# Optimization experiments

Measured on AMD Instinct MI355X. Metric: run time of the kernel, lower is better.

The kernel has to match this reference:

```python
import jax, jax.numpy as jnp
import numpy as np

N_NODES = 100000
N_EDGES = 1600000
IN_CH = 128
OUT_CH = 128


def setup_inputs() -> dict:
    key = jax.random.key(0)
    k1, k2, k3 = jax.random.split(key, 3)
    x = jax.random.normal(k1, (N_NODES, IN_CH), dtype=jnp.float32)
    edge_index = jax.random.randint(k2, (2, N_EDGES), 0, N_NODES, dtype=jnp.int64)
    # glorot-like init for the linear weight, stored as [in, out]
    W = jax.random.normal(k3, (IN_CH, OUT_CH), dtype=jnp.float32) * (2.0 / (IN_CH + OUT_CH)) ** 0.5
    bias = jnp.zeros((OUT_CH,), dtype=jnp.float32)
    return {"x": x, "edge_index": edge_index, "W": W, "bias": bias}


def reference(x, edge_index, W, bias):
    N = x.shape[0]
    # linear transform (bias-free, matches Linear(in, out, bias=False))
    h = x @ W  # [N, out]

    # add self loops (improved=False -> fill_value = 1.0)
    loop = jnp.arange(N, dtype=edge_index.dtype)
    src = jnp.concatenate([edge_index[0], loop])
    dst = jnp.concatenate([edge_index[1], loop])
    ew = jnp.ones(src.shape[0], dtype=h.dtype)  # edge_weight None -> ones

    # symmetric GCN normalization: deg from dst, norm = d^-1/2[src] * w * d^-1/2[dst]
    deg = jax.ops.segment_sum(ew, dst, num_segments=N)
    deg_inv_sqrt = jnp.where(deg > 0, jax.lax.rsqrt(deg), 0.0)
    w = deg_inv_sqrt[src] * ew * deg_inv_sqrt[dst]

    # spmm aggregation: out[dst] += w * h[src]
    out = jax.ops.segment_sum(h[src] * w[:, None], dst, num_segments=N)
    return out + bias
```

## Files before the change

kernel.cpp:

```cpp
#include <hip/hip_runtime.h>
#include <hip/hip_bf16.h>

constexpr int kNodes = 100000;
constexpr int kEdges = 1600000;
constexpr int kCh    = 128;
constexpr int kCap   = 32;
constexpr int kOvfCap = 8192;
constexpr int kPartSize = kNodes / 8;
constexpr int kFillBlocks = 512;
constexpr int kGemmBlocks = (kNodes + 127) / 128;

typedef __attribute__((ext_vector_type(8))) short short8;
typedef __attribute__((ext_vector_type(4))) float floatx4;
typedef __attribute__((ext_vector_type(4))) int   intx4;
typedef __attribute__((ext_vector_type(2))) float floatx2;


__global__ __launch_bounds__(512) void k_fused(const float* __restrict__ x,
                                               const float* __restrict__ W,
                                               const int* __restrict__ srcArr,
                                               const int* __restrict__ dstArr,
                                               int* __restrict__ cnt,
                                               int* __restrict__ bucket,
                                               int* __restrict__ ovfCnt,
                                               int* __restrict__ ovfD,
                                               int* __restrict__ ovfS,
                                               __hip_bfloat16* __restrict__ hs) {
  if (blockIdx.x < kFillBlocks) {
    int part = blockIdx.x & 7;
    int bip  = blockIdx.x >> 3;
    int lo = part * kPartSize;
    const intx4* d4 = (const intx4*)dstArr;
    const intx4* s4 = (const intx4*)srcArr;
    for (int i = bip * 512 + (int)threadIdx.x; i < kEdges / 4; i += (kFillBlocks >> 3) * 512) {
      intx4 dv = __builtin_nontemporal_load(d4 + i);
      intx4 sv = __builtin_nontemporal_load(s4 + i);
      #pragma unroll
      for (int k = 0; k < 4; k++) {
        int d = dv[k];
        if ((unsigned)(d - lo) < (unsigned)kPartSize) {
          int pos = atomicAdd(&cnt[d], 1);
          if (pos < kCap) {
            bucket[(long)d * kCap + pos] = sv[k];
          } else {
            int o = atomicAdd(ovfCnt, 1);
            if (o < kOvfCap) { ovfD[o] = d; ovfS[o] = sv[k]; }
          }
        }
      }
    }
    return;
  }

  __shared__ short8 Bf[2048];
  for (int e = threadIdx.x; e < 2048; e += 512) {
    int lane = e & 63, c = (e >> 6) & 3, tt = e >> 8;
    int quad = lane >> 4, mcol = lane & 15;
    short8 v;
    #pragma unroll
    for (int j = 0; j < 8; j++) {
      __hip_bfloat16 h = __float2bfloat16(W[(c * 32 + quad * 8 + j) * kCh + tt * 16 + mcol]);
      v[j] = *(short*)&h;
    }
    Bf[e] = v;
  }
  __syncthreads();

  int wave = threadIdx.x >> 6;
  int lane = threadIdx.x & 63;
  int quad = lane >> 4;
  int mcol = lane & 15;
  int gb = blockIdx.x - kFillBlocks;
  long rowBase = ((long)gb * 8 + wave) * 16;
  if (rowBase >= kNodes) return;

  long arow = rowBase + mcol;
  if (arow >= kNodes) arow = kNodes - 1;
  const float* xp = x + arow * kCh;
  short8 afrag[4];
  #pragma unroll
  for (int c = 0; c < 4; c++) {
    const floatx4* p = (const floatx4*)(xp + c * 32 + quad * 8);
    floatx4 v0 = __builtin_nontemporal_load(p);
    floatx4 v1 = __builtin_nontemporal_load(p + 1);
    #pragma unroll
    for (int j = 0; j < 4; j++) {
      __hip_bfloat16 h0 = __float2bfloat16(v0[j]);
      __hip_bfloat16 h1 = __float2bfloat16(v1[j]);
      afrag[c][j]     = *(short*)&h0;
      afrag[c][j + 4] = *(short*)&h1;
    }
  }

  #pragma unroll
  for (int t = 0; t < 8; t++) {
    floatx4 acc = {0.f, 0.f, 0.f, 0.f};
    #pragma unroll
    for (int c = 0; c < 4; c++) {
      short8 b = Bf[(t * 4 + c) * 64 + lane];
      acc = __builtin_amdgcn_mfma_f32_16x16x32_bf16(afrag[c], b, acc, 0, 0, 0);
    }
    #pragma unroll
    for (int i = 0; i < 4; i++) {
      long r = rowBase + quad * 4 + i;
      if (r < kNodes) {
        __hip_bfloat16 h = __float2bfloat16(acc[i]);
        __builtin_nontemporal_store(*(short*)&h, (short*)hs + r * kCh + t * 16 + mcol);
      }
    }
  }
}


__global__ __launch_bounds__(256) void k_aggregate(const int* __restrict__ cnt,
                                                   const int* __restrict__ bucket,
                                                   const int* __restrict__ ovfCnt,
                                                   const int* __restrict__ ovfD,
                                                   const int* __restrict__ ovfS,
                                                   const __hip_bfloat16* __restrict__ hs,
                                                   const float* __restrict__ bias,
                                                   float* __restrict__ out) {
  int gid  = blockIdx.x * 256 + threadIdx.x;
  int node = gid >> 6;
  int lane = gid & 63;
  if (node >= kNodes) return;

  const __hip_bfloat162* hbase = (const __hip_bfloat162*)hs;

  int degRaw = cnt[node];
  float dd = rsqrtf((float)(degRaw + 1));

  float2 sf = __bfloat1622float2(hbase[(long)node * (kCh / 2) + lane]);
  float acc0 = dd * sf.x;
  float acc1 = dd * sf.y;

  int c = degRaw < kCap ? degRaw : kCap;
  const int* bkt = bucket + (long)node * kCap;

  int j = 0;
  for (; j + 7 < c; j += 8) {
    int s[8];
    #pragma unroll
    for (int u = 0; u < 8; u++) s[u] = __builtin_nontemporal_load(bkt + j + u);
    int cs[8];
    #pragma unroll
    for (int u = 0; u < 8; u++) cs[u] = cnt[s[u]];
    __hip_bfloat162 v[8];
    #pragma unroll
    for (int u = 0; u < 8; u++) v[u] = hbase[(long)s[u] * (kCh / 2) + lane];
    #pragma unroll
    for (int u = 0; u < 8; u++) {
      float dv = rsqrtf((float)(cs[u] + 1));
      float2 f = __bfloat1622float2(v[u]);
      acc0 = fmaf(dv, f.x, acc0);
      acc1 = fmaf(dv, f.y, acc1);
    }
  }
  for (; j < c; ++j) {
    int s = __builtin_nontemporal_load(bkt + j);
    float dv = rsqrtf((float)(cnt[s] + 1));
    float2 f = __bfloat1622float2(hbase[(long)s * (kCh / 2) + lane]);
    acc0 = fmaf(dv, f.x, acc0);
    acc1 = fmaf(dv, f.y, acc1);
  }

  if (degRaw > kCap) {
    int n = *ovfCnt;
    if (n > kOvfCap) n = kOvfCap;
    for (int i = 0; i < n; i++) {
      if (ovfD[i] == node) {
        int s = ovfS[i];
        float dv = rsqrtf((float)(cnt[s] + 1));
        float2 f = __bfloat1622float2(hbase[(long)s * (kCh / 2) + lane]);
        acc0 = fmaf(dv, f.x, acc0);
        acc1 = fmaf(dv, f.y, acc1);
      }
    }
  }

  float2 b = ((const float2*)bias)[lane];
  floatx2 o;
  o[0] = dd * acc0 + b.x;
  o[1] = dd * acc1 + b.y;
  __builtin_nontemporal_store(o, (floatx2*)(out + (long)node * kCh) + lane);
}


extern "C" void kernel_launch(void* const* d_in, const int* in_sizes, int n_in,
                              void* d_out, int out_size, void* d_ws, size_t ws_size,
                              hipStream_t stream) {
  const float* x    = (const float*)d_in[0];
  const int*   ei   = (const int*)d_in[1];
  const float* W    = (const float*)d_in[2];
  const float* bias = (const float*)d_in[3];
  float* out = (float*)d_out;

  const int* srcArr = ei;
  const int* dstArr = ei + kEdges;

  char* ws = (char*)d_ws;
  size_t off = 0;
  __hip_bfloat16* hs = (__hip_bfloat16*)(ws + off); off += (size_t)kNodes * kCh * 2;
  int*   bucket  = (int*)  (ws + off); off += (size_t)kNodes * kCap * 4;
  int*   cnt     = (int*)  (ws + off); off += (size_t)kNodes * 4;
  int*   ovfCnt  = (int*)  (ws + off); off += 128;
  int*   ovfD    = (int*)  (ws + off); off += (size_t)kOvfCap * 4;
  int*   ovfS    = (int*)  (ws + off); off += (size_t)kOvfCap * 4;

  (void)hipMemsetAsync(cnt, 0, (size_t)kNodes * 4 + 128, stream);

  k_fused<<<kFillBlocks + kGemmBlocks, 512, 0, stream>>>(x, W, srcArr, dstArr, cnt, bucket,
                                                         ovfCnt, ovfD, ovfS, hs);

  long aggThreads = (long)kNodes * 64;
  int gAgg = (int)((aggThreads + 255) / 256);
  k_aggregate<<<gAgg, 256, 0, stream>>>(cnt, bucket, ovfCnt, ovfD, ovfS, hs, bias, out);
}
```

Before: 284.9 us.

## Bin edges by destination partition before bucket fill and precompute degree inverse

Replaces the fill step, where every block scanned all edges and filtered by partition, with a two-pass scheme. The first pass reads each edge once and uses wave ballots to append it to a per-partition, per-XCD segment. A separate fill kernel then does the per-node bucket atomics from those segments, and the last block of each partition writes a precomputed rsqrt degree array. The aggregate kernel reads dinv instead of recomputing rsqrt from cnt, and drops its nontemporal hints. This adds a kernel launch and extra segment traffic, and the fixed segment capacity could overflow on skewed inputs.

```diff
diff --git a/kernel.cpp b/kernel.cpp
--- a/kernel.cpp
+++ b/kernel.cpp
@@ -7,45 +7,61 @@
 constexpr int kCap   = 32;
 constexpr int kOvfCap = 8192;
 constexpr int kPartSize = kNodes / 8;
+constexpr int kBinBlocks = 128;
+constexpr int kGemmBlocks = (kNodes + 127) / 128;
+constexpr int kSegCap = 28672;
 constexpr int kFillBlocks = 512;
-constexpr int kGemmBlocks = (kNodes + 127) / 128;
 
 typedef __attribute__((ext_vector_type(8))) short short8;
 typedef __attribute__((ext_vector_type(4))) float floatx4;
 typedef __attribute__((ext_vector_type(4))) int   intx4;
-typedef __attribute__((ext_vector_type(2))) float floatx2;
-
-
-__global__ __launch_bounds__(512) void k_fused(const float* __restrict__ x,
-                                               const float* __restrict__ W,
-                                               const int* __restrict__ srcArr,
-                                               const int* __restrict__ dstArr,
-                                               int* __restrict__ cnt,
-                                               int* __restrict__ bucket,
-                                               int* __restrict__ ovfCnt,
-                                               int* __restrict__ ovfD,
-                                               int* __restrict__ ovfS,
-                                               __hip_bfloat16* __restrict__ hs) {
-  if (blockIdx.x < kFillBlocks) {
-    int part = blockIdx.x & 7;
-    int bip  = blockIdx.x >> 3;
-    int lo = part * kPartSize;
+
+
+__global__ __launch_bounds__(512) void k_bin_gemm(const float* __restrict__ x,
+                                                  const float* __restrict__ W,
+                                                  const int* __restrict__ srcArr,
+                                                  const int* __restrict__ dstArr,
+                                                  long* __restrict__ segs,
+                                                  int* __restrict__ segCnt,
+                                                  __hip_bfloat16* __restrict__ hs) {
+  if (blockIdx.x < kBinBlocks) {
+    int lane = threadIdx.x & 63;
+    int xcd  = blockIdx.x & 7;
     const intx4* d4 = (const intx4*)dstArr;
     const intx4* s4 = (const intx4*)srcArr;
-    for (int i = bip * 512 + (int)threadIdx.x; i < kEdges / 4; i += (kFillBlocks >> 3) * 512) {
-      intx4 dv = __builtin_nontemporal_load(d4 + i);
-      intx4 sv = __builtin_nontemporal_load(s4 + i);
+    constexpr int nQuads = kEdges / 4;
+    constexpr int stride = kBinBlocks * 512;
+    constexpr int rounds = (nQuads + stride - 1) / stride;
+    unsigned long long lt = (1ull << lane) - 1;
+    int i = blockIdx.x * 512 + threadIdx.x;
+    for (int r = 0; r < rounds; r++, i += stride) {
+      bool valid = i < nQuads;
+      intx4 dv = {0, 0, 0, 0}, sv = {0, 0, 0, 0};
+      if (valid) {
+        dv = __builtin_nontemporal_load(d4 + i);
+        sv = __builtin_nontemporal_load(s4 + i);
+      }
+      int part[4];
       #pragma unroll
-      for (int k = 0; k < 4; k++) {
-        int d = dv[k];
-        if ((unsigned)(d - lo) < (unsigned)kPartSize) {
-          int pos = atomicAdd(&cnt[d], 1);
-          if (pos < kCap) {
-            bucket[(long)d * kCap + pos] = sv[k];
-          } else {
-            int o = atomicAdd(ovfCnt, 1);
-            if (o < kOvfCap) { ovfD[o] = d; ovfS[o] = sv[k]; }
+      for (int k = 0; k < 4; k++) part[k] = valid ? (dv[k] / kPartSize) : 8;
+      for (int p = 0; p < 8; p++) {
+        unsigned long long m[4];
+        #pragma unroll
+        for (int k = 0; k < 4; k++) m[k] = __ballot(part[k] == p);
+        int tot = __popcll(m[0]) + __popcll(m[1]) + __popcll(m[2]) + __popcll(m[3]);
+        if (tot == 0) continue;
+        int base = 0;
+        if (lane == 0) base = atomicAdd(&segCnt[(p * 8 + xcd) * 32], tot);
+        base = __shfl(base, 0, 64);
+        long* seg = segs + (long)(p * 8 + xcd) * kSegCap;
+        int run = base;
+        #pragma unroll
+        for (int k = 0; k < 4; k++) {
+          if (part[k] == p) {
+            long e = ((long)dv[k] << 32) | (unsigned)sv[k];
+            seg[run + __popcll(m[k] & lt)] = e;
           }
+          run += __popcll(m[k]);
         }
       }
     }
@@ -70,7 +86,7 @@
   int lane = threadIdx.x & 63;
   int quad = lane >> 4;
   int mcol = lane & 15;
-  int gb = blockIdx.x - kFillBlocks;
+  int gb = blockIdx.x - kBinBlocks;
   long rowBase = ((long)gb * 8 + wave) * 16;
   if (rowBase >= kNodes) return;
 
@@ -112,8 +128,53 @@
 }
 
 
+__global__ __launch_bounds__(256) void k_fill(const long* __restrict__ segs,
+                                              const int* __restrict__ segCnt,
+                                              int* __restrict__ cnt,
+                                              int* __restrict__ bucket,
+                                              int* __restrict__ ovfCnt,
+                                              int* __restrict__ ovfD,
+                                              int* __restrict__ ovfS,
+                                              int* __restrict__ partDone,
+                                              float* __restrict__ dinv) {
+  int p   = blockIdx.x & 7;
+  int sub = blockIdx.x >> 3;
+  for (int xs = 0; xs < 8; xs++) {
+    int n = segCnt[(p * 8 + xs) * 32];
+    if (n > kSegCap) n = kSegCap;
+    const long* seg = segs + (long)(p * 8 + xs) * kSegCap;
+    for (int i = sub * 256 + (int)threadIdx.x; i < n; i += 64 * 256) {
+      long e = seg[i];
+      int s = (int)(e & 0xffffffffL);
+      int d = (int)(e >> 32);
+      int pos = atomicAdd(&cnt[d], 1);
+      if (pos < kCap) {
+        bucket[(long)d * kCap + pos] = s;
+      } else {
+        int o = atomicAdd(ovfCnt, 1);
+        if (o < kOvfCap) { ovfD[o] = d; ovfS[o] = s; }
+      }
+    }
+  }
+
+  __shared__ int lastFlag;
+  __threadfence();
+  __syncthreads();
+  if (threadIdx.x == 0) lastFlag = (atomicAdd(&partDone[p * 32], 1) == 63);
+  __syncthreads();
+  if (lastFlag) {
+    int lo = p * kPartSize;
+    for (int i = threadIdx.x; i < kPartSize; i += 256) {
+      int c = atomicAdd(&cnt[lo + i], 0);
+      dinv[lo + i] = rsqrtf((float)(c + 1));
+    }
+  }
+}
+
+
 __global__ __launch_bounds__(256) void k_aggregate(const int* __restrict__ cnt,
                                                    const int* __restrict__ bucket,
+                                                   const float* __restrict__ dinv,
                                                    const int* __restrict__ ovfCnt,
                                                    const int* __restrict__ ovfD,
                                                    const int* __restrict__ ovfS,
@@ -128,7 +189,7 @@
   const __hip_bfloat162* hbase = (const __hip_bfloat162*)hs;
 
   int degRaw = cnt[node];
-  float dd = rsqrtf((float)(degRaw + 1));
+  float dd = dinv[node];
 
   float2 sf = __bfloat1622float2(hbase[(long)node * (kCh / 2) + lane]);
   float acc0 = dd * sf.x;
@@ -141,24 +202,23 @@
   for (; j + 7 < c; j += 8) {
     int s[8];
     #pragma unroll
-    for (int u = 0; u < 8; u++) s[u] = __builtin_nontemporal_load(bkt + j + u);
-    int cs[8];
-    #pragma unroll
-    for (int u = 0; u < 8; u++) cs[u] = cnt[s[u]];
+    for (int u = 0; u < 8; u++) s[u] = bkt[j + u];
+    float dv[8];
+    #pragma unroll
+    for (int u = 0; u < 8; u++) dv[u] = dinv[s[u]];
     __hip_bfloat162 v[8];
     #pragma unroll
     for (int u = 0; u < 8; u++) v[u] = hbase[(long)s[u] * (kCh / 2) + lane];
     #pragma unroll
     for (int u = 0; u < 8; u++) {
-      float dv = rsqrtf((float)(cs[u] + 1));
       float2 f = __bfloat1622float2(v[u]);
-      acc0 = fmaf(dv, f.x, acc0);
-      acc1 = fmaf(dv, f.y, acc1);
+      acc0 = fmaf(dv[u], f.x, acc0);
+      acc1 = fmaf(dv[u], f.y, acc1);
     }
   }
   for (; j < c; ++j) {
-    int s = __builtin_nontemporal_load(bkt + j);
-    float dv = rsqrtf((float)(cnt[s] + 1));
+    int s = bkt[j];
+    float dv = dinv[s];
     float2 f = __bfloat1622float2(hbase[(long)s * (kCh / 2) + lane]);
     acc0 = fmaf(dv, f.x, acc0);
     acc1 = fmaf(dv, f.y, acc1);
@@ -170,19 +230,18 @@
     for (int i = 0; i < n; i++) {
       if (ovfD[i] == node) {
         int s = ovfS[i];
-        float dv = rsqrtf((float)(cnt[s] + 1));
         float2 f = __bfloat1622float2(hbase[(long)s * (kCh / 2) + lane]);
-        acc0 = fmaf(dv, f.x, acc0);
-        acc1 = fmaf(dv, f.y, acc1);
+        acc0 = fmaf(dinv[s], f.x, acc0);
+        acc1 = fmaf(dinv[s], f.y, acc1);
       }
     }
   }
 
   float2 b = ((const float2*)bias)[lane];
-  floatx2 o;
-  o[0] = dd * acc0 + b.x;
-  o[1] = dd * acc1 + b.y;
-  __builtin_nontemporal_store(o, (floatx2*)(out + (long)node * kCh) + lane);
+  float2 o;
+  o.x = dd * acc0 + b.x;
+  o.y = dd * acc1 + b.y;
+  ((float2*)(out + (long)node * kCh))[lane] = o;
 }
 
 
@@ -202,17 +261,27 @@
   size_t off = 0;
   __hip_bfloat16* hs = (__hip_bfloat16*)(ws + off); off += (size_t)kNodes * kCh * 2;
   int*   bucket  = (int*)  (ws + off); off += (size_t)kNodes * kCap * 4;
-  int*   cnt     = (int*)  (ws + off); off += (size_t)kNodes * 4;
-  int*   ovfCnt  = (int*)  (ws + off); off += 128;
-  int*   ovfD    = (int*)  (ws + off); off += (size_t)kOvfCap * 4;
-  int*   ovfS    = (int*)  (ws + off); off += (size_t)kOvfCap * 4;
-
-  (void)hipMemsetAsync(cnt, 0, (size_t)kNodes * 4 + 128, stream);
-
-  k_fused<<<kFillBlocks + kGemmBlocks, 512, 0, stream>>>(x, W, srcArr, dstArr, cnt, bucket,
-                                                         ovfCnt, ovfD, ovfS, hs);
+  long*  segs    = (long*) (ws + off); off += (size_t)64 * kSegCap * 8;
+  float* dinv    = (float*)(ws + off); off += (size_t)kNodes * 4;
+  char* zbase = ws + off;
+  int*   cnt      = (int*)(ws + off); off += (size_t)kNodes * 4;
+  int*   segCnt   = (int*)(ws + off); off += 64 * 32 * 4;
+  int*   partDone = (int*)(ws + off); off += 8 * 32 * 4;
+  int*   ovfCnt   = (int*)(ws + off); off += 128;
+  size_t zbytes = (size_t)((ws + off) - zbase);
+  int*   ovfD     = (int*)(ws + off); off += (size_t)kOvfCap * 4;
+  int*   ovfS     = (int*)(ws + off); off += (size_t)kOvfCap * 4;
+
+  (void)hipMemsetAsync(zbase, 0, zbytes, stream);
+
+  k_bin_gemm<<<kBinBlocks + kGemmBlocks, 512, 0, stream>>>(x, W, srcArr, dstArr,
+                                                           segs, segCnt, hs);
+
+  k_fill<<<kFillBlocks, 256, 0, stream>>>(segs, segCnt, cnt, bucket,
+                                          ovfCnt, ovfD, ovfS, partDone, dinv);
 
   long aggThreads = (long)kNodes * 64;
   int gAgg = (int)((aggThreads + 255) / 256);
-  k_aggregate<<<gAgg, 256, 0, stream>>>(cnt, bucket, ovfCnt, ovfD, ovfS, hs, bias, out);
-}
+  k_aggregate<<<gAgg, 256, 0, stream>>>(cnt, bucket, dinv, ovfCnt, ovfD, ovfS,
+                                        hs, bias, out);
+}
```

After: 407.9 us. 1.43x slower.
